# Performance work log

Measured on AMD Instinct MI355X. Metric: run time of the kernel, lower is better.

Reference implementation:

```python
import jax, jax.numpy as jnp
import numpy as np

B, T, V, H, L = 128, 512, 256, 512, 2  # batch, seq, vocab, hidden, layers


def setup_inputs() -> dict:
    key = jax.random.key(0)
    ks = jax.random.split(key, 12)
    s = 0.05
    p = lambda k, shape: (jax.random.normal(k, shape, jnp.float32) * s)
    return {
        "x": jax.random.normal(ks[0], (B, T, V), jnp.float32),
        # layer 0 (input size V)
        "w_ih0": p(ks[1], (4 * H, V)),
        "w_hh0": p(ks[2], (4 * H, H)),
        "b_ih0": p(ks[3], (4 * H,)),
        "b_hh0": p(ks[4], (4 * H,)),
        # layer 1 (input size H)
        "w_ih1": p(ks[5], (4 * H, H)),
        "w_hh1": p(ks[6], (4 * H, H)),
        "b_ih1": p(ks[7], (4 * H,)),
        "b_hh1": p(ks[8], (4 * H,)),
        # final projection
        "fc_w": p(ks[9], (V, H)),
        "fc_b": p(ks[10], (V,)),
    }


def _lstm_layer(x, w_ih, w_hh, b_ih, b_hh):
    """x: [B,T,in] -> (outputs [B,T,H], h_T [B,H], c_T [B,H]). PyTorch gate order i,f,g,o."""
    Bb = x.shape[0]
    Hh = w_hh.shape[1]
    # precompute input contribution for all timesteps: [B,T,4H]
    pre = jnp.einsum('bti,gi->btg', x, w_ih) + b_ih + b_hh

    def step(carry, xt):
        h, c = carry
        gates = xt + h @ w_hh.T  # [B,4H]
        i, f, g, o = jnp.split(gates, 4, axis=-1)
        i = jax.nn.sigmoid(i)
        f = jax.nn.sigmoid(f)
        g = jnp.tanh(g)
        o = jax.nn.sigmoid(o)
        c = f * c + i * g
        h = o * jnp.tanh(c)
        return (h, c), h

    h0 = jnp.zeros((Bb, Hh), x.dtype)
    (hT, cT), hs = jax.lax.scan(step, (h0, h0), jnp.swapaxes(pre, 0, 1))
    return jnp.swapaxes(hs, 0, 1), hT, cT


def reference(x, w_ih0, w_hh0, b_ih0, b_hh0, w_ih1, w_hh1, b_ih1, b_hh1, fc_w, fc_b):
    out0, h0, c0 = _lstm_layer(x, w_ih0, w_hh0, b_ih0, b_hh0)
    out1, h1, c1 = _lstm_layer(out0, w_ih1, w_hh1, b_ih1, b_hh1)
    last = out1[:, -1, :]                # slice final timestep [B,H]
    # dropout is identity in eval mode
    logits = last @ fc_w.T + fc_b        # [B,V]
    h_n = jnp.stack([h0, h1])            # [L,B,H]
    c_n = jnp.stack([c0, c1])
    return (logits, h_n, c_n)
```

## Files before the change

### kernel.cpp

```cpp
#include <hip/hip_runtime.h>
#include <math.h>

#define B_ 128
#define T_ 512
#define V_ 256
#define H_ 512

typedef unsigned short u16;
typedef unsigned int u32;
typedef unsigned long long u64;
typedef __attribute__((ext_vector_type(8))) __bf16 bf16x8;
typedef __attribute__((ext_vector_type(4))) float f32x4;
typedef __attribute__((ext_vector_type(4))) u32 u32x4;

__device__ __forceinline__ float sigf(float x) { return 1.f / (1.f + __expf(-x)); }
__device__ __forceinline__ float tanh_fast(float x) {
    x = fminf(fmaxf(x, -15.f), 15.f);
    float e = __expf(2.f * x);
    return (e - 1.f) / (e + 1.f);
}
__device__ __forceinline__ u16 f2bf(float f) {
    union { float f; u32 u; } v; v.f = f;
    u32 r = v.u + 0x7FFFu + ((v.u >> 16) & 1u);
    return (u16)(r >> 16);
}

__device__ __forceinline__ u64 aload(const u64* p) {
    return __hip_atomic_load(p, __ATOMIC_RELAXED, __HIP_MEMORY_SCOPE_AGENT);
}
__device__ __forceinline__ void astore(u64* p, u64 v) {
    __hip_atomic_store(p, v, __ATOMIC_RELAXED, __HIP_MEMORY_SCOPE_AGENT);
}
__device__ __forceinline__ u32 aload32(const u32* p) {
    return __hip_atomic_load(p, __ATOMIC_RELAXED, __HIP_MEMORY_SCOPE_AGENT);
}
__device__ __forceinline__ void astore32(u32* p, u32 v) {
    __hip_atomic_store(p, v, __ATOMIC_RELAXED, __HIP_MEMORY_SCOPE_AGENT);
}
__device__ __forceinline__ void pollge(const u32* slots, int idx, int target) {
    const u32* p = slots + idx;
    for (;;) {
        u32 v = aload32(p);
        if (__all((int)v >= target)) break;
        __builtin_amdgcn_s_sleep(1);
    }
    __builtin_amdgcn_sched_barrier(0);
    asm volatile("" ::: "memory");
}
__device__ __forceinline__ bf16x8 afrag(const u16* p) {
    union { u64 d[2]; bf16x8 v; } u;
    u.d[0] = aload((const u64*)p);
    u.d[1] = aload((const u64*)(p + 4));
    return u.v;
}

__global__ __launch_bounds__(256) void conv_x(u16* __restrict__ dst, const float* __restrict__ x) {
    int tid = blockIdx.x * 256 + threadIdx.x;
    int k = tid & (V_ - 1);
    int t = (tid >> 8) & (T_ - 1);
    int b = tid >> 17;
    float v = x[tid];
    int lane = (b & 15) | (((k >> 3) & 3) << 4);
    dst[((((size_t)t * 8 + (b >> 4)) * 8) + (k >> 5)) * 512 + (size_t)lane * 8 + (k & 7)] = f2bf(v);
}

__global__ __launch_bounds__(256) void conv_w(u16* __restrict__ dst,
                                              const float* __restrict__ wih,
                                              const float* __restrict__ whh,
                                              int KIN, int Ktot) {
    int tid = blockIdx.x * 256 + threadIdx.x;
    int n = tid / Ktot, k = tid - n * Ktot;
    float v = (k < KIN) ? wih[(size_t)n * KIN + k] : whh[(size_t)n * H_ + (k - KIN)];
    int lane = (n & 15) | (((k >> 3) & 3) << 4);
    dst[((size_t)((n >> 4) * (Ktot >> 5) + (k >> 5))) * 512 + (size_t)lane * 8 + (k & 7)] = f2bf(v);
}

__global__ __launch_bounds__(256) void vadd(float* __restrict__ d,
                                            const float* __restrict__ a,
                                            const float* __restrict__ b, int n) {
    int i = blockIdx.x * 256 + threadIdx.x;
    if (i < n) d[i] = a[i] + b[i];
}


template <int LAYER>
__device__ __forceinline__ void run_loop(
    const u16* __restrict__ Xswz, u16* __restrict__ Out0,
    const u16* __restrict__ WBs,
    f32x4* __restrict__ scr,
    u16* __restrict__ tileb,
    u32* __restrict__ Hgrp,
    const float* __restrict__ bsum, float* __restrict__ out,
    u32* __restrict__ bc,
    int js, int mq, int wid, int lane)
{
    constexpr int KCA = LAYER ? 16 : 8;
    constexpr int KCT = KCA + 16;
    const int m = wid & 1;
    const bool isA = wid < 2;
    const int jl = (js << 4) | (lane & 15);

    if (isA) {
        for (int s = -1; s < T_; ++s) {
            const int tc = s + 1;
            if (tc < T_) {
                f32x4 acc[4];
                #pragma unroll
                for (int g = 0; g < 4; ++g) acc[g] = (f32x4){0.f, 0.f, 0.f, 0.f};
                if (LAYER == 0) {
                    const u16* As = Xswz + (size_t)tc * 32768 + (size_t)(2 * mq + m) * 4096 + (size_t)lane * 8;
                    #pragma unroll
                    for (int kc = 0; kc < 8; ++kc) {
                        bf16x8 a = *(const bf16x8*)(As + (size_t)kc * 512);
                        #pragma unroll
                        for (int g = 0; g < 4; ++g)
                            acc[g] = __builtin_amdgcn_mfma_f32_16x16x32_bf16(
                                a, *(const bf16x8*)(WBs + (size_t)(g * KCT + kc) * 512 + (size_t)lane * 8), acc[g], 0, 0, 0);
                    }
                } else {
                    pollge(bc + m * 32, lane & 31, tc + 1);
                    const u16* As = Out0 + (size_t)tc * 65536 + (size_t)(2 * mq + m) * 8192 + (size_t)lane * 8;
                    bf16x8 fa[16];
                    #pragma unroll
                    for (int kc = 0; kc < 16; ++kc) fa[kc] = afrag(As + (size_t)kc * 512);
                    #pragma unroll
                    for (int kc = 0; kc < 16; ++kc) {
                        #pragma unroll
                        for (int g = 0; g < 4; ++g)
                            acc[g] = __builtin_amdgcn_mfma_f32_16x16x32_bf16(
                                fa[kc], *(const bf16x8*)(WBs + (size_t)(g * KCT + kc) * 512 + (size_t)lane * 8), acc[g], 0, 0, 0);
                    }
                }
                #pragma unroll
                for (int g = 0; g < 4; ++g) scr[(size_t)(((tc & 1) * 2 + m) * 4 + g) * 64 + lane] = acc[g];
            }
            __syncthreads();
        }
    } else {
        const float bi0 = bsum[jl], bi1 = bsum[512 + jl];
        const float bi2 = bsum[1024 + jl], bi3 = bsum[1536 + jl];
        f32x4 creg = {0.f, 0.f, 0.f, 0.f};
        u32* bcs = bc + m * 32 + js;

        for (int s = -1; s < T_; ++s) {
            if (s >= 0) {
                const u32 tag = (u32)s;
                const u32* hb = Hgrp + (size_t)(tag & 1) * 16384 + (size_t)m * 8192;

                f32x4 acc[4];
                #pragma unroll
                for (int g = 0; g < 4; ++g) acc[g] = scr[(size_t)(((s & 1) * 2 + m) * 4 + g) * 64 + lane];

                u64 fa[16], fb[16];
                #pragma unroll
                for (int i = 0; i < 16; ++i)
                    fa[i] = aload((const u64*)(hb + (size_t)(i >> 2) * 512 + (size_t)lane * 8) + (i & 3));

                #pragma unroll
                for (int c = 0; c < 4; ++c) {
                    u64* cur = (c & 1) ? fb : fa;
                    u64* nxt = (c & 1) ? fa : fb;
                    if (c < 3) {
                        #pragma unroll
                        for (int i = 0; i < 16; ++i)
                            nxt[i] = aload((const u64*)(hb + (size_t)((c + 1) * 4 + (i >> 2)) * 512 + (size_t)lane * 8) + (i & 3));
                    }
                    for (;;) {
                        u32 bad = 0u;
                        #pragma unroll
                        for (int i = 0; i < 16; ++i) bad |= (((u32)(cur[i] >> 16)) & 0xFFFFu) ^ tag;
                        if (!__any(bad != 0u)) break;
                        #pragma unroll
                        for (int i = 0; i < 16; ++i)
                            cur[i] = aload((const u64*)(hb + (size_t)(c * 4 + (i >> 2)) * 512 + (size_t)lane * 8) + (i & 3));
                    }
                    #pragma unroll
                    for (int k2 = 0; k2 < 4; ++k2) {
                        const u64 g0 = cur[4 * k2 + 0], g1 = cur[4 * k2 + 1];
                        const u64 g2 = cur[4 * k2 + 2], g3 = cur[4 * k2 + 3];
                        u32 w0 = (u32)(g0 & 0xFFFFu) | ((u32)(g0 >> 32) << 16);
                        u32 w1 = (u32)(g1 & 0xFFFFu) | ((u32)(g1 >> 32) << 16);
                        u32 w2 = (u32)(g2 & 0xFFFFu) | ((u32)(g2 >> 32) << 16);
                        u32 w3 = (u32)(g3 & 0xFFFFu) | ((u32)(g3 >> 32) << 16);
                        u32x4 ww = {w0, w1, w2, w3};
                        bf16x8 a = __builtin_bit_cast(bf16x8, ww);
                        const int kc = 4 * c + k2;
                        #pragma unroll
                        for (int g = 0; g < 4; ++g)
                            acc[g] = __builtin_amdgcn_mfma_f32_16x16x32_bf16(
                                a, *(const bf16x8*)(WBs + (size_t)(g * KCT + KCA + kc) * 512 + (size_t)lane * 8), acc[g], 0, 0, 0);
                    }
                }

                if (LAYER == 0 && s >= 1) {
                    asm volatile("s_waitcnt vmcnt(0)" ::: "memory");
                    if (lane == 0) astore32(bcs, (u32)s);
                }

                const bool is_last = (s == T_ - 1);
                const int bb = (lane >> 4) << 2;
                #pragma unroll
                for (int r = 0; r < 4; ++r) {
                    const float vi = sigf(acc[0][r] + bi0);
                    const float vf = sigf(acc[1][r] + bi1);
                    const float vg = tanh_fast(acc[2][r] + bi2);
                    const float vo = sigf(acc[3][r] + bi3);
                    const float cn = vf * creg[r] + vi * vg;
                    creg[r] = cn;
                    const float hn = vo * tanh_fast(cn);
                    tileb[(size_t)(m * 16 + bb + r) * 20 + (lane & 15)] = f2bf(hn);
                    if (is_last) {
                        const int bg = mq * 32 + m * 16 + bb + r;
                        out[(LAYER ? 98304 : 32768) + bg * 512 + jl] = hn;
                        out[(LAYER ? 229376 : 163840) + bg * 512 + jl] = cn;
                    }
                }
                const u32 wtag = (u32)(s + 1);
                u32* hw = Hgrp + (size_t)(wtag & 1) * 16384 + (size_t)m * 8192;
                #pragma unroll
                for (int q = 0; q < 2; ++q) {
                    u32 w = *(const u32*)&tileb[(size_t)(m * 16 + (lane >> 2)) * 20 + q * 8 + (lane & 3) * 2];
                    u64 v = (u64)(w & 0xFFFFu) | ((u64)wtag << 16)
                          | ((u64)(w >> 16) << 32) | ((u64)wtag << 48);
                    astore((u64*)(hw + (size_t)(js >> 1) * 512 + (size_t)((js & 1) * 2 + q) * 128
                                  + (size_t)(lane >> 2) * 8 + (size_t)((lane & 3) * 2)), v);
                }
                if (LAYER == 0) {
                    const int q2 = lane >> 5, lw = lane & 31, b2 = lw >> 1, e4 = (lw & 1) * 4;
                    u64 v = *(const u64*)&tileb[(size_t)(m * 16 + b2) * 20 + q2 * 8 + e4];
                    astore((u64*)(Out0 + (size_t)s * 65536 + (size_t)(2 * mq + m) * 8192
                                  + (size_t)(js >> 1) * 512 + (size_t)((js & 1) * 2 + q2) * 128
                                  + (size_t)b2 * 8 + (size_t)e4), v);
                }
            }
            __syncthreads();
        }
        if (LAYER == 0) {
            asm volatile("s_waitcnt vmcnt(0)" ::: "memory");
            if (lane == 0) astore32(bcs, (u32)(T_ + 1));
        }
    }
}

__global__ __launch_bounds__(256, 1) void lstm_persistent(
    const u16* __restrict__ Xswz, u16* __restrict__ Out0swz,
    const u16* __restrict__ WB0, const u16* __restrict__ WB1,
    const float* __restrict__ bsum0, const float* __restrict__ bsum1,
    u32* __restrict__ Htag, float* __restrict__ out, u32* __restrict__ bc)
{
    __shared__ u16 WBs[4 * 32 * 512];
    __shared__ f32x4 scr[2 * 2 * 4 * 64];
    __shared__ __align__(16) u16 tileb[2 * 16 * 20];

    const int bid = blockIdx.x;
    const int g = bid & 7, js = bid >> 3;
    const int layer = g >> 2, mq = g & 3;
    const int tid = threadIdx.x;
    const int wid = tid >> 6, lane = tid & 63;

    const int KCtot = layer ? 32 : 24;
    const u16* WB = layer ? WB1 : WB0;
    for (int gg = 0; gg < 4; ++gg) {
        const u32x4* s4 = (const u32x4*)(WB + ((size_t)(gg * 32 + js) * KCtot) * 512);
        u32x4* d4 = (u32x4*)(WBs + (size_t)gg * KCtot * 512);
        for (int i = tid; i < KCtot * 64; i += 256) d4[i] = s4[i];
    }
    __syncthreads();

    u32* Hgrp = Htag + (size_t)g * 32768;
    u32* bcg = bc + mq * 64;

    if (layer == 0)
        run_loop<0>(Xswz, Out0swz, WBs, scr, tileb, Hgrp, bsum0, out, bcg, js, mq, wid, lane);
    else
        run_loop<1>(Xswz, Out0swz, WBs, scr, tileb, Hgrp, bsum1, out, bcg, js, mq, wid, lane);
}

__device__ __forceinline__ float dot4_(float4 a, float4 w, float s) {
    s = fmaf(a.x, w.x, s); s = fmaf(a.y, w.y, s);
    s = fmaf(a.z, w.z, s); s = fmaf(a.w, w.w, s);
    return s;
}

__global__ __launch_bounds__(256) void logits_kernel(
    const float* __restrict__ h1, const float* __restrict__ fc_w,
    const float* __restrict__ fc_b, float* __restrict__ out)
{
    __shared__ float hs[H_];
    const int b = blockIdx.x;
    for (int k = threadIdx.x; k < H_; k += 256) hs[k] = h1[(size_t)b * H_ + k];
    __syncthreads();
    const int v = threadIdx.x;
    const float4* wr = reinterpret_cast<const float4*>(fc_w + (size_t)v * H_);
    const float4* hr = reinterpret_cast<const float4*>(hs);
    float s = 0.f;
    #pragma unroll 8
    for (int k = 0; k < H_ / 4; ++k) s = dot4_(hr[k], wr[k], s);
    out[(size_t)b * V_ + v] = s + fc_b[v];
}

extern "C" void kernel_launch(void* const* d_in, const int* in_sizes, int n_in,
                              void* d_out, int out_size, void* d_ws, size_t ws_size,
                              hipStream_t stream) {
    const float* x     = (const float*)d_in[0];
    const float* w_ih0 = (const float*)d_in[1];
    const float* w_hh0 = (const float*)d_in[2];
    const float* b_ih0 = (const float*)d_in[3];
    const float* b_hh0 = (const float*)d_in[4];
    const float* w_ih1 = (const float*)d_in[5];
    const float* w_hh1 = (const float*)d_in[6];
    const float* b_ih1 = (const float*)d_in[7];
    const float* b_hh1 = (const float*)d_in[8];
    const float* fc_w  = (const float*)d_in[9];
    const float* fc_b  = (const float*)d_in[10];
    float* out = (float*)d_out;

    char* p = (char*)d_ws;
    u16* Xswz    = (u16*)p; p += (size_t)512 * 32768 * 2;
    u16* Out0swz = (u16*)p; p += (size_t)512 * 65536 * 2;
    u16* WB0     = (u16*)p; p += (size_t)128 * 24 * 512 * 2;
    u16* WB1     = (u16*)p; p += (size_t)128 * 32 * 512 * 2;
    u32* Htag    = (u32*)p; p += (size_t)8 * 32768 * 4;
    float* bsum0 = (float*)p; p += 2048 * 4;
    float* bsum1 = (float*)p; p += 2048 * 4;
    u32* bc      = (u32*)p;  p += 4 * 64 * 4;

    hipMemsetAsync(Htag, 0, (size_t)8 * 32768 * 4, stream);
    hipMemsetAsync(bc, 0, 4 * 64 * 4, stream);
    conv_x<<<65536, 256, 0, stream>>>(Xswz, x);
    conv_w<<<(2048 * 768) / 256, 256, 0, stream>>>(WB0, w_ih0, w_hh0, 256, 768);
    conv_w<<<(2048 * 1024) / 256, 256, 0, stream>>>(WB1, w_ih1, w_hh1, 512, 1024);
    vadd<<<8, 256, 0, stream>>>(bsum0, b_ih0, b_hh0, 2048);
    vadd<<<8, 256, 0, stream>>>(bsum1, b_ih1, b_hh1, 2048);

    lstm_persistent<<<256, 256, 0, stream>>>(
        Xswz, Out0swz, WB0, WB1, bsum0, bsum1, Htag, out, bc);

    logits_kernel<<<B_, 256, 0, stream>>>(out + 98304, fc_w, fc_b, out);
}
```

Baseline: 2.682 ms.

## Merge input-projection waves into recurrent waves and drop per-step block barrier

Removes the separate producer waves that computed the input projection one step ahead into shared scratch, along with the __syncthreads per timestep. Each recurrent wave now computes the next step's input contribution itself, straight after storing h, so blocks shrink from 256 to 128 threads. This takes the block-wide barrier off the serial critical path. The cost is that input-projection MFMAs now run serially within each wave instead of in parallel on separate waves. The s_waitcnt before the layer-0 progress-flag store is also removed, which may weaken the ordering between the Out0 stores and the flag that layer 1 polls.

```diff
diff --git a/kernel.cpp b/kernel.cpp
--- a/kernel.cpp
+++ b/kernel.cpp
@@ -87,183 +87,186 @@
 __device__ __forceinline__ void run_loop(
     const u16* __restrict__ Xswz, u16* __restrict__ Out0,
     const u16* __restrict__ WBs,
-    f32x4* __restrict__ scr,
     u16* __restrict__ tileb,
     u32* __restrict__ Hgrp,
     const float* __restrict__ bsum, float* __restrict__ out,
     u32* __restrict__ bc,
-    int js, int mq, int wid, int lane)
+    int js, int mq, int m, int lane)
 {
     constexpr int KCA = LAYER ? 16 : 8;
     constexpr int KCT = KCA + 16;
-    const int m = wid & 1;
-    const bool isA = wid < 2;
     const int jl = (js << 4) | (lane & 15);
-
-    if (isA) {
-        for (int s = -1; s < T_; ++s) {
-            const int tc = s + 1;
-            if (tc < T_) {
-                f32x4 acc[4];
-                #pragma unroll
-                for (int g = 0; g < 4; ++g) acc[g] = (f32x4){0.f, 0.f, 0.f, 0.f};
-                if (LAYER == 0) {
-                    const u16* As = Xswz + (size_t)tc * 32768 + (size_t)(2 * mq + m) * 4096 + (size_t)lane * 8;
+    const float bi0 = bsum[jl], bi1 = bsum[512 + jl];
+    const float bi2 = bsum[1024 + jl], bi3 = bsum[1536 + jl];
+    f32x4 creg = {0.f, 0.f, 0.f, 0.f};
+    u32* bcs = bc + m * 32 + js;
+    const u32* bcp = bc + m * 32;
+
+    f32x4 acc[4];
+    #pragma unroll
+    for (int g = 0; g < 4; ++g) acc[g] = (f32x4){0.f, 0.f, 0.f, 0.f};
+
+    if (LAYER == 0) {
+        const u16* As = Xswz + (size_t)(2 * mq + m) * 4096 + (size_t)lane * 8;
+        #pragma unroll
+        for (int kc = 0; kc < 8; ++kc) {
+            bf16x8 a = *(const bf16x8*)(As + (size_t)kc * 512);
+            #pragma unroll
+            for (int g = 0; g < 4; ++g)
+                acc[g] = __builtin_amdgcn_mfma_f32_16x16x32_bf16(
+                    a, *(const bf16x8*)(WBs + (size_t)(g * KCT + kc) * 512 + (size_t)lane * 8), acc[g], 0, 0, 0);
+        }
+    } else {
+        pollge(bcp, lane & 31, 1);
+        const u16* As = Out0 + (size_t)(2 * mq + m) * 8192 + (size_t)lane * 8;
+        #pragma unroll
+        for (int kc = 0; kc < 16; ++kc) {
+            bf16x8 a = afrag(As + (size_t)kc * 512);
+            #pragma unroll
+            for (int g = 0; g < 4; ++g)
+                acc[g] = __builtin_amdgcn_mfma_f32_16x16x32_bf16(
+                    a, *(const bf16x8*)(WBs + (size_t)(g * KCT + kc) * 512 + (size_t)lane * 8), acc[g], 0, 0, 0);
+        }
+    }
+
+    for (int s = 0; s < T_; ++s) {
+        const u32 tag = (u32)s;
+        const u32* hb = Hgrp + (size_t)(s & 1) * 16384 + (size_t)m * 8192;
+        u64 fA[16], fB[16];
+        #pragma unroll
+        for (int i = 0; i < 16; ++i)
+            fA[i] = aload((const u64*)(hb + (size_t)(i >> 2) * 512 + (size_t)lane * 8) + (i & 3));
+
+        #pragma unroll
+        for (int c = 0; c < 4; ++c) {
+            u64* cur = (c & 1) ? fB : fA;
+            u64* nxt = (c & 1) ? fA : fB;
+            if (c < 3) {
+                #pragma unroll
+                for (int i = 0; i < 16; ++i)
+                    nxt[i] = aload((const u64*)(hb + (size_t)((c + 1) * 4 + (i >> 2)) * 512 + (size_t)lane * 8) + (i & 3));
+            }
+            for (;;) {
+                u32 bad = 0u;
+                #pragma unroll
+                for (int i = 0; i < 16; ++i) bad |= (((u32)(cur[i] >> 16)) & 0xFFFFu) ^ tag;
+                if (!__any(bad != 0u)) break;
+                #pragma unroll
+                for (int i = 0; i < 16; ++i)
+                    cur[i] = aload((const u64*)(hb + (size_t)(c * 4 + (i >> 2)) * 512 + (size_t)lane * 8) + (i & 3));
+            }
+            #pragma unroll
+            for (int k2 = 0; k2 < 4; ++k2) {
+                const u64 g0 = cur[4 * k2 + 0], g1 = cur[4 * k2 + 1];
+                const u64 g2 = cur[4 * k2 + 2], g3 = cur[4 * k2 + 3];
+                u32 w0 = (u32)(g0 & 0xFFFFu) | ((u32)(g0 >> 32) << 16);
+                u32 w1 = (u32)(g1 & 0xFFFFu) | ((u32)(g1 >> 32) << 16);
+                u32 w2 = (u32)(g2 & 0xFFFFu) | ((u32)(g2 >> 32) << 16);
+                u32 w3 = (u32)(g3 & 0xFFFFu) | ((u32)(g3 >> 32) << 16);
+                u32x4 ww = {w0, w1, w2, w3};
+                bf16x8 a = __builtin_bit_cast(bf16x8, ww);
+                const int kc = 4 * c + k2;
+                #pragma unroll
+                for (int g = 0; g < 4; ++g)
+                    acc[g] = __builtin_amdgcn_mfma_f32_16x16x32_bf16(
+                        a, *(const bf16x8*)(WBs + (size_t)(g * KCT + KCA + kc) * 512 + (size_t)lane * 8), acc[g], 0, 0, 0);
+            }
+        }
+
+        if (LAYER == 0 && s >= 1 && lane == 0) astore32(bcs, (u32)s);
+
+        const bool is_last = (s == T_ - 1);
+        const int bb = (lane >> 4) << 2;
+        #pragma unroll
+        for (int r = 0; r < 4; ++r) {
+            const float vi = sigf(acc[0][r] + bi0);
+            const float vf = sigf(acc[1][r] + bi1);
+            const float vg = tanh_fast(acc[2][r] + bi2);
+            const float vo = sigf(acc[3][r] + bi3);
+            const float cn = vf * creg[r] + vi * vg;
+            creg[r] = cn;
+            const float hn = vo * tanh_fast(cn);
+            tileb[(size_t)(m * 16 + bb + r) * 20 + (lane & 15)] = f2bf(hn);
+            if (is_last) {
+                const int bg = mq * 32 + m * 16 + bb + r;
+                out[(LAYER ? 98304 : 32768) + bg * 512 + jl] = hn;
+                out[(LAYER ? 229376 : 163840) + bg * 512 + jl] = cn;
+            }
+        }
+
+        const u32 wtag = (u32)(s + 1);
+        u32* hw = Hgrp + (size_t)((s + 1) & 1) * 16384 + (size_t)m * 8192;
+        #pragma unroll
+        for (int q = 0; q < 2; ++q) {
+            u32 w = *(const u32*)&tileb[(size_t)(m * 16 + (lane >> 2)) * 20 + q * 8 + (lane & 3) * 2];
+            u64 v = (u64)(w & 0xFFFFu) | ((u64)wtag << 16)
+                  | ((u64)(w >> 16) << 32) | ((u64)wtag << 48);
+            astore((u64*)(hw + (size_t)(js >> 1) * 512 + (size_t)((js & 1) * 2 + q) * 128
+                          + (size_t)(lane >> 2) * 8 + (size_t)((lane & 3) * 2)), v);
+        }
+        if (LAYER == 0) {
+            const int q2 = lane >> 5, lw = lane & 31, b2 = lw >> 1, e4 = (lw & 1) * 4;
+            u64 v = *(const u64*)&tileb[(size_t)(m * 16 + b2) * 20 + q2 * 8 + e4];
+            astore((u64*)(Out0 + (size_t)s * 65536 + (size_t)(2 * mq + m) * 8192
+                          + (size_t)(js >> 1) * 512 + (size_t)((js & 1) * 2 + q2) * 128
+                          + (size_t)b2 * 8 + (size_t)e4), v);
+        }
+
+        #pragma unroll
+        for (int g = 0; g < 4; ++g) acc[g] = (f32x4){0.f, 0.f, 0.f, 0.f};
+        if (s + 1 < T_) {
+            if (LAYER == 0) {
+                const u16* As = Xswz + (size_t)(s + 1) * 32768 + (size_t)(2 * mq + m) * 4096 + (size_t)lane * 8;
+                #pragma unroll
+                for (int kc = 0; kc < 8; ++kc) {
+                    bf16x8 a = *(const bf16x8*)(As + (size_t)kc * 512);
                     #pragma unroll
-                    for (int kc = 0; kc < 8; ++kc) {
-                        bf16x8 a = *(const bf16x8*)(As + (size_t)kc * 512);
-                        #pragma unroll
-                        for (int g = 0; g < 4; ++g)
-                            acc[g] = __builtin_amdgcn_mfma_f32_16x16x32_bf16(
-                                a, *(const bf16x8*)(WBs + (size_t)(g * KCT + kc) * 512 + (size_t)lane * 8), acc[g], 0, 0, 0);
-                    }
-                } else {
-                    pollge(bc + m * 32, lane & 31, tc + 1);
-                    const u16* As = Out0 + (size_t)tc * 65536 + (size_t)(2 * mq + m) * 8192 + (size_t)lane * 8;
-                    bf16x8 fa[16];
+                    for (int g = 0; g < 4; ++g)
+                        acc[g] = __builtin_amdgcn_mfma_f32_16x16x32_bf16(
+                            a, *(const bf16x8*)(WBs + (size_t)(g * KCT + kc) * 512 + (size_t)lane * 8), acc[g], 0, 0, 0);
+                }
+            } else {
+                pollge(bcp, lane & 31, s + 2);
+                const u16* As = Out0 + (size_t)(s + 1) * 65536 + (size_t)(2 * mq + m) * 8192 + (size_t)lane * 8;
+                #pragma unroll
+                for (int kc = 0; kc < 16; ++kc) {
+                    bf16x8 a = afrag(As + (size_t)kc * 512);
                     #pragma unroll
-                    for (int kc = 0; kc < 16; ++kc) fa[kc] = afrag(As + (size_t)kc * 512);
-                    #pragma unroll
-                    for (int kc = 0; kc < 16; ++kc) {
-                        #pragma unroll
-                        for (int g = 0; g < 4; ++g)
-                            acc[g] = __builtin_amdgcn_mfma_f32_16x16x32_bf16(
-                                fa[kc], *(const bf16x8*)(WBs + (size_t)(g * KCT + kc) * 512 + (size_t)lane * 8), acc[g], 0, 0, 0);
-                    }
+                    for (int g = 0; g < 4; ++g)
+                        acc[g] = __builtin_amdgcn_mfma_f32_16x16x32_bf16(
+                            a, *(const bf16x8*)(WBs + (size_t)(g * KCT + kc) * 512 + (size_t)lane * 8), acc[g], 0, 0, 0);
                 }
-                #pragma unroll
-                for (int g = 0; g < 4; ++g) scr[(size_t)(((tc & 1) * 2 + m) * 4 + g) * 64 + lane] = acc[g];
-            }
-            __syncthreads();
-        }
-    } else {
-        const float bi0 = bsum[jl], bi1 = bsum[512 + jl];
-        const float bi2 = bsum[1024 + jl], bi3 = bsum[1536 + jl];
-        f32x4 creg = {0.f, 0.f, 0.f, 0.f};
-        u32* bcs = bc + m * 32 + js;
-
-        for (int s = -1; s < T_; ++s) {
-            if (s >= 0) {
-                const u32 tag = (u32)s;
-                const u32* hb = Hgrp + (size_t)(tag & 1) * 16384 + (size_t)m * 8192;
-
-                f32x4 acc[4];
-                #pragma unroll
-                for (int g = 0; g < 4; ++g) acc[g] = scr[(size_t)(((s & 1) * 2 + m) * 4 + g) * 64 + lane];
-
-                u64 fa[16], fb[16];
-                #pragma unroll
-                for (int i = 0; i < 16; ++i)
-                    fa[i] = aload((const u64*)(hb + (size_t)(i >> 2) * 512 + (size_t)lane * 8) + (i & 3));
-
-                #pragma unroll
-                for (int c = 0; c < 4; ++c) {
-                    u64* cur = (c & 1) ? fb : fa;
-                    u64* nxt = (c & 1) ? fa : fb;
-                    if (c < 3) {
-                        #pragma unroll
-                        for (int i = 0; i < 16; ++i)
-                            nxt[i] = aload((const u64*)(hb + (size_t)((c + 1) * 4 + (i >> 2)) * 512 + (size_t)lane * 8) + (i & 3));
-                    }
-                    for (;;) {
-                        u32 bad = 0u;
-                        #pragma unroll
-                        for (int i = 0; i < 16; ++i) bad |= (((u32)(cur[i] >> 16)) & 0xFFFFu) ^ tag;
-                        if (!__any(bad != 0u)) break;
-                        #pragma unroll
-                        for (int i = 0; i < 16; ++i)
-                            cur[i] = aload((const u64*)(hb + (size_t)(c * 4 + (i >> 2)) * 512 + (size_t)lane * 8) + (i & 3));
-                    }
-                    #pragma unroll
-                    for (int k2 = 0; k2 < 4; ++k2) {
-                        const u64 g0 = cur[4 * k2 + 0], g1 = cur[4 * k2 + 1];
-                        const u64 g2 = cur[4 * k2 + 2], g3 = cur[4 * k2 + 3];
-                        u32 w0 = (u32)(g0 & 0xFFFFu) | ((u32)(g0 >> 32) << 16);
-                        u32 w1 = (u32)(g1 & 0xFFFFu) | ((u32)(g1 >> 32) << 16);
-                        u32 w2 = (u32)(g2 & 0xFFFFu) | ((u32)(g2 >> 32) << 16);
-                        u32 w3 = (u32)(g3 & 0xFFFFu) | ((u32)(g3 >> 32) << 16);
-                        u32x4 ww = {w0, w1, w2, w3};
-                        bf16x8 a = __builtin_bit_cast(bf16x8, ww);
-                        const int kc = 4 * c + k2;
-                        #pragma unroll
-                        for (int g = 0; g < 4; ++g)
-                            acc[g] = __builtin_amdgcn_mfma_f32_16x16x32_bf16(
-                                a, *(const bf16x8*)(WBs + (size_t)(g * KCT + KCA + kc) * 512 + (size_t)lane * 8), acc[g], 0, 0, 0);
-                    }
-                }
-
-                if (LAYER == 0 && s >= 1) {
-                    asm volatile("s_waitcnt vmcnt(0)" ::: "memory");
-                    if (lane == 0) astore32(bcs, (u32)s);
-                }
-
-                const bool is_last = (s == T_ - 1);
-                const int bb = (lane >> 4) << 2;
-                #pragma unroll
-                for (int r = 0; r < 4; ++r) {
-                    const float vi = sigf(acc[0][r] + bi0);
-                    const float vf = sigf(acc[1][r] + bi1);
-                    const float vg = tanh_fast(acc[2][r] + bi2);
-                    const float vo = sigf(acc[3][r] + bi3);
-                    const float cn = vf * creg[r] + vi * vg;
-                    creg[r] = cn;
-                    const float hn = vo * tanh_fast(cn);
-                    tileb[(size_t)(m * 16 + bb + r) * 20 + (lane & 15)] = f2bf(hn);
-                    if (is_last) {
-                        const int bg = mq * 32 + m * 16 + bb + r;
-                        out[(LAYER ? 98304 : 32768) + bg * 512 + jl] = hn;
-                        out[(LAYER ? 229376 : 163840) + bg * 512 + jl] = cn;
-                    }
-                }
-                const u32 wtag = (u32)(s + 1);
-                u32* hw = Hgrp + (size_t)(wtag & 1) * 16384 + (size_t)m * 8192;
-                #pragma unroll
-                for (int q = 0; q < 2; ++q) {
-                    u32 w = *(const u32*)&tileb[(size_t)(m * 16 + (lane >> 2)) * 20 + q * 8 + (lane & 3) * 2];
-                    u64 v = (u64)(w & 0xFFFFu) | ((u64)wtag << 16)
-                          | ((u64)(w >> 16) << 32) | ((u64)wtag << 48);
-                    astore((u64*)(hw + (size_t)(js >> 1) * 512 + (size_t)((js & 1) * 2 + q) * 128
-                                  + (size_t)(lane >> 2) * 8 + (size_t)((lane & 3) * 2)), v);
-                }
-                if (LAYER == 0) {
-                    const int q2 = lane >> 5, lw = lane & 31, b2 = lw >> 1, e4 = (lw & 1) * 4;
-                    u64 v = *(const u64*)&tileb[(size_t)(m * 16 + b2) * 20 + q2 * 8 + e4];
-                    astore((u64*)(Out0 + (size_t)s * 65536 + (size_t)(2 * mq + m) * 8192
-                                  + (size_t)(js >> 1) * 512 + (size_t)((js & 1) * 2 + q2) * 128
-                                  + (size_t)b2 * 8 + (size_t)e4), v);
-                }
-            }
-            __syncthreads();
-        }
-        if (LAYER == 0) {
-            asm volatile("s_waitcnt vmcnt(0)" ::: "memory");
-            if (lane == 0) astore32(bcs, (u32)(T_ + 1));
-        }
-    }
-}
-
-__global__ __launch_bounds__(256, 1) void lstm_persistent(
+            }
+        }
+    }
+
+    if (LAYER == 0) {
+        asm volatile("s_waitcnt vmcnt(0)" ::: "memory");
+        if (lane == 0) astore32(bcs, (u32)(T_ + 1));
+    }
+}
+
+__global__ __launch_bounds__(128, 1) void lstm_persistent(
     const u16* __restrict__ Xswz, u16* __restrict__ Out0swz,
     const u16* __restrict__ WB0, const u16* __restrict__ WB1,
     const float* __restrict__ bsum0, const float* __restrict__ bsum1,
     u32* __restrict__ Htag, float* __restrict__ out, u32* __restrict__ bc)
 {
     __shared__ u16 WBs[4 * 32 * 512];
-    __shared__ f32x4 scr[2 * 2 * 4 * 64];
     __shared__ __align__(16) u16 tileb[2 * 16 * 20];
 
     const int bid = blockIdx.x;
     const int g = bid & 7, js = bid >> 3;
     const int layer = g >> 2, mq = g & 3;
     const int tid = threadIdx.x;
-    const int wid = tid >> 6, lane = tid & 63;
+    const int m = tid >> 6, lane = tid & 63;
 
     const int KCtot = layer ? 32 : 24;
     const u16* WB = layer ? WB1 : WB0;
     for (int gg = 0; gg < 4; ++gg) {
         const u32x4* s4 = (const u32x4*)(WB + ((size_t)(gg * 32 + js) * KCtot) * 512);
         u32x4* d4 = (u32x4*)(WBs + (size_t)gg * KCtot * 512);
-        for (int i = tid; i < KCtot * 64; i += 256) d4[i] = s4[i];
+        for (int i = tid; i < KCtot * 64; i += 128) d4[i] = s4[i];
     }
     __syncthreads();
 
@@ -271,9 +274,9 @@
     u32* bcg = bc + mq * 64;
 
     if (layer == 0)
-        run_loop<0>(Xswz, Out0swz, WBs, scr, tileb, Hgrp, bsum0, out, bcg, js, mq, wid, lane);
+        run_loop<0>(Xswz, Out0swz, WBs, tileb, Hgrp, bsum0, out, bcg, js, mq, m, lane);
     else
-        run_loop<1>(Xswz, Out0swz, WBs, scr, tileb, Hgrp, bsum1, out, bcg, js, mq, wid, lane);
+        run_loop<1>(Xswz, Out0swz, WBs, tileb, Hgrp, bsum1, out, bcg, js, mq, m, lane);
 }
 
 __device__ __forceinline__ float dot4_(float4 a, float4 w, float s) {
@@ -333,7 +336,7 @@
     vadd<<<8, 256, 0, stream>>>(bsum0, b_ih0, b_hh0, 2048);
     vadd<<<8, 256, 0, stream>>>(bsum1, b_ih1, b_hh1, 2048);
 
-    lstm_persistent<<<256, 256, 0, stream>>>(
+    lstm_persistent<<<256, 128, 0, stream>>>(
         Xswz, Out0swz, WB0, WB1, bsum0, bsum1, Htag, out, bc);
 
     logits_kernel<<<B_, 256, 0, stream>>>(out + 98304, fc_w, fc_b, out);
```

Measured after the change: 5.098 ms. 1.9x slower.

## Replace block-wide barriers with LDS mailbox flags between producer and consumer waves

Applied to the files above, without the earlier changes.

The per-timestep __syncthreads that coupled the input-projection waves and the recurrent waves is replaced by LDS mailbox counters. Each producer/consumer pair now handshakes point-to-point through a two-slot buffer, which lets the input projection run up to one step ahead without stalling all four waves. The recurrent waves also issue their first h loads before waiting on the mailbox, and the vmcnt wait before the layer-0 progress store is removed. The risks are spin-wait overhead and memory-ordering hazards, since the progress flag can now be published before the Out0 stores have completed.

```diff
diff --git a/kernel.cpp b/kernel.cpp
--- a/kernel.cpp
+++ b/kernel.cpp
@@ -89,6 +89,7 @@
     const u16* __restrict__ WBs,
     f32x4* __restrict__ scr,
     u16* __restrict__ tileb,
+    volatile u32* __restrict__ mbox,
     u32* __restrict__ Hgrp,
     const float* __restrict__ bsum, float* __restrict__ out,
     u32* __restrict__ bc,
@@ -101,40 +102,42 @@
     const int jl = (js << 4) | (lane & 15);
 
     if (isA) {
-        for (int s = -1; s < T_; ++s) {
-            const int tc = s + 1;
-            if (tc < T_) {
-                f32x4 acc[4];
+        for (int tc = 0; tc < T_; ++tc) {
+            while ((int)mbox[2 + m] < tc - 1) __builtin_amdgcn_s_sleep(1);
+            __builtin_amdgcn_sched_barrier(0);
+            asm volatile("" ::: "memory");
+
+            f32x4 acc[4];
+            #pragma unroll
+            for (int g = 0; g < 4; ++g) acc[g] = (f32x4){0.f, 0.f, 0.f, 0.f};
+            if (LAYER == 0) {
+                const u16* As = Xswz + (size_t)tc * 32768 + (size_t)(2 * mq + m) * 4096 + (size_t)lane * 8;
                 #pragma unroll
-                for (int g = 0; g < 4; ++g) acc[g] = (f32x4){0.f, 0.f, 0.f, 0.f};
-                if (LAYER == 0) {
-                    const u16* As = Xswz + (size_t)tc * 32768 + (size_t)(2 * mq + m) * 4096 + (size_t)lane * 8;
-                    #pragma unroll
-                    for (int kc = 0; kc < 8; ++kc) {
-                        bf16x8 a = *(const bf16x8*)(As + (size_t)kc * 512);
-                        #pragma unroll
-                        for (int g = 0; g < 4; ++g)
-                            acc[g] = __builtin_amdgcn_mfma_f32_16x16x32_bf16(
-                                a, *(const bf16x8*)(WBs + (size_t)(g * KCT + kc) * 512 + (size_t)lane * 8), acc[g], 0, 0, 0);
-                    }
-                } else {
-                    pollge(bc + m * 32, lane & 31, tc + 1);
-                    const u16* As = Out0 + (size_t)tc * 65536 + (size_t)(2 * mq + m) * 8192 + (size_t)lane * 8;
-                    bf16x8 fa[16];
-                    #pragma unroll
-                    for (int kc = 0; kc < 16; ++kc) fa[kc] = afrag(As + (size_t)kc * 512);
-                    #pragma unroll
-                    for (int kc = 0; kc < 16; ++kc) {
-                        #pragma unroll
-                        for (int g = 0; g < 4; ++g)
-                            acc[g] = __builtin_amdgcn_mfma_f32_16x16x32_bf16(
-                                fa[kc], *(const bf16x8*)(WBs + (size_t)(g * KCT + kc) * 512 + (size_t)lane * 8), acc[g], 0, 0, 0);
-                    }
-                }
+                for (int kc = 0; kc < 8; ++kc) {
+                    bf16x8 a = *(const bf16x8*)(As + (size_t)kc * 512);
+                    #pragma unroll
+                    for (int g = 0; g < 4; ++g)
+                        acc[g] = __builtin_amdgcn_mfma_f32_16x16x32_bf16(
+                            a, *(const bf16x8*)(WBs + (size_t)(g * KCT + kc) * 512 + (size_t)lane * 8), acc[g], 0, 0, 0);
+                }
+            } else {
+                pollge(bc + m * 32, lane & 31, tc + 1);
+                const u16* As = Out0 + (size_t)tc * 65536 + (size_t)(2 * mq + m) * 8192 + (size_t)lane * 8;
+                bf16x8 fa[16];
                 #pragma unroll
-                for (int g = 0; g < 4; ++g) scr[(size_t)(((tc & 1) * 2 + m) * 4 + g) * 64 + lane] = acc[g];
-            }
-            __syncthreads();
+                for (int kc = 0; kc < 16; ++kc) fa[kc] = afrag(As + (size_t)kc * 512);
+                #pragma unroll
+                for (int kc = 0; kc < 16; ++kc) {
+                    #pragma unroll
+                    for (int g = 0; g < 4; ++g)
+                        acc[g] = __builtin_amdgcn_mfma_f32_16x16x32_bf16(
+                            fa[kc], *(const bf16x8*)(WBs + (size_t)(g * KCT + kc) * 512 + (size_t)lane * 8), acc[g], 0, 0, 0);
+                }
+            }
+            #pragma unroll
+            for (int g = 0; g < 4; ++g) scr[(size_t)(((tc & 1) * 2 + m) * 4 + g) * 64 + lane] = acc[g];
+            asm volatile("s_waitcnt lgkmcnt(0)" ::: "memory");
+            if (lane == 0) mbox[m] = (u32)(tc + 1);
         }
     } else {
         const float bi0 = bsum[jl], bi1 = bsum[512 + jl];
@@ -142,98 +145,96 @@
         f32x4 creg = {0.f, 0.f, 0.f, 0.f};
         u32* bcs = bc + m * 32 + js;
 
-        for (int s = -1; s < T_; ++s) {
-            if (s >= 0) {
-                const u32 tag = (u32)s;
-                const u32* hb = Hgrp + (size_t)(tag & 1) * 16384 + (size_t)m * 8192;
-
-                f32x4 acc[4];
+        for (int s = 0; s < T_; ++s) {
+            const u32 tag = (u32)s;
+            const u32* hb = Hgrp + (size_t)(s & 1) * 16384 + (size_t)m * 8192;
+            u64 fA[16], fB[16];
+            #pragma unroll
+            for (int i = 0; i < 16; ++i)
+                fA[i] = aload((const u64*)(hb + (size_t)(i >> 2) * 512 + (size_t)lane * 8) + (i & 3));
+
+            while ((int)mbox[m] < s + 1) __builtin_amdgcn_s_sleep(1);
+            __builtin_amdgcn_sched_barrier(0);
+            asm volatile("" ::: "memory");
+            f32x4 acc[4];
+            #pragma unroll
+            for (int g = 0; g < 4; ++g) acc[g] = scr[(size_t)(((s & 1) * 2 + m) * 4 + g) * 64 + lane];
+            asm volatile("s_waitcnt lgkmcnt(0)" ::: "memory");
+            if (lane == 0) mbox[2 + m] = (u32)(s + 1);
+
+            #pragma unroll
+            for (int c = 0; c < 4; ++c) {
+                u64* cur = (c & 1) ? fB : fA;
+                u64* nxt = (c & 1) ? fA : fB;
+                if (c < 3) {
+                    #pragma unroll
+                    for (int i = 0; i < 16; ++i)
+                        nxt[i] = aload((const u64*)(hb + (size_t)((c + 1) * 4 + (i >> 2)) * 512 + (size_t)lane * 8) + (i & 3));
+                }
+                for (;;) {
+                    u32 bad = 0u;
+                    #pragma unroll
+                    for (int i = 0; i < 16; ++i) bad |= (((u32)(cur[i] >> 16)) & 0xFFFFu) ^ tag;
+                    if (!__any(bad != 0u)) break;
+                    #pragma unroll
+                    for (int i = 0; i < 16; ++i)
+                        cur[i] = aload((const u64*)(hb + (size_t)(c * 4 + (i >> 2)) * 512 + (size_t)lane * 8) + (i & 3));
+                }
                 #pragma unroll
-                for (int g = 0; g < 4; ++g) acc[g] = scr[(size_t)(((s & 1) * 2 + m) * 4 + g) * 64 + lane];
-
-                u64 fa[16], fb[16];
-                #pragma unroll
-                for (int i = 0; i < 16; ++i)
-                    fa[i] = aload((const u64*)(hb + (size_t)(i >> 2) * 512 + (size_t)lane * 8) + (i & 3));
-
-                #pragma unroll
-                for (int c = 0; c < 4; ++c) {
-                    u64* cur = (c & 1) ? fb : fa;
-                    u64* nxt = (c & 1) ? fa : fb;
-                    if (c < 3) {
-                        #pragma unroll
-                        for (int i = 0; i < 16; ++i)
-                            nxt[i] = aload((const u64*)(hb + (size_t)((c + 1) * 4 + (i >> 2)) * 512 + (size_t)lane * 8) + (i & 3));
-                    }
-                    for (;;) {
-                        u32 bad = 0u;
-                        #pragma unroll
-                        for (int i = 0; i < 16; ++i) bad |= (((u32)(cur[i] >> 16)) & 0xFFFFu) ^ tag;
-                        if (!__any(bad != 0u)) break;
-                        #pragma unroll
-                        for (int i = 0; i < 16; ++i)
-                            cur[i] = aload((const u64*)(hb + (size_t)(c * 4 + (i >> 2)) * 512 + (size_t)lane * 8) + (i & 3));
-                    }
-                    #pragma unroll
-                    for (int k2 = 0; k2 < 4; ++k2) {
-                        const u64 g0 = cur[4 * k2 + 0], g1 = cur[4 * k2 + 1];
-                        const u64 g2 = cur[4 * k2 + 2], g3 = cur[4 * k2 + 3];
-                        u32 w0 = (u32)(g0 & 0xFFFFu) | ((u32)(g0 >> 32) << 16);
-                        u32 w1 = (u32)(g1 & 0xFFFFu) | ((u32)(g1 >> 32) << 16);
-                        u32 w2 = (u32)(g2 & 0xFFFFu) | ((u32)(g2 >> 32) << 16);
-                        u32 w3 = (u32)(g3 & 0xFFFFu) | ((u32)(g3 >> 32) << 16);
-                        u32x4 ww = {w0, w1, w2, w3};
-                        bf16x8 a = __builtin_bit_cast(bf16x8, ww);
-                        const int kc = 4 * c + k2;
-                        #pragma unroll
-                        for (int g = 0; g < 4; ++g)
-                            acc[g] = __builtin_amdgcn_mfma_f32_16x16x32_bf16(
-                                a, *(const bf16x8*)(WBs + (size_t)(g * KCT + KCA + kc) * 512 + (size_t)lane * 8), acc[g], 0, 0, 0);
-                    }
-                }
-
-                if (LAYER == 0 && s >= 1) {
-                    asm volatile("s_waitcnt vmcnt(0)" ::: "memory");
-                    if (lane == 0) astore32(bcs, (u32)s);
-                }
-
-                const bool is_last = (s == T_ - 1);
-                const int bb = (lane >> 4) << 2;
-                #pragma unroll
-                for (int r = 0; r < 4; ++r) {
-                    const float vi = sigf(acc[0][r] + bi0);
-                    const float vf = sigf(acc[1][r] + bi1);
-                    const float vg = tanh_fast(acc[2][r] + bi2);
-                    const float vo = sigf(acc[3][r] + bi3);
-                    const float cn = vf * creg[r] + vi * vg;
-                    creg[r] = cn;
-                    const float hn = vo * tanh_fast(cn);
-                    tileb[(size_t)(m * 16 + bb + r) * 20 + (lane & 15)] = f2bf(hn);
-                    if (is_last) {
-                        const int bg = mq * 32 + m * 16 + bb + r;
-                        out[(LAYER ? 98304 : 32768) + bg * 512 + jl] = hn;
-                        out[(LAYER ? 229376 : 163840) + bg * 512 + jl] = cn;
-                    }
-                }
-                const u32 wtag = (u32)(s + 1);
-                u32* hw = Hgrp + (size_t)(wtag & 1) * 16384 + (size_t)m * 8192;
-                #pragma unroll
-                for (int q = 0; q < 2; ++q) {
-                    u32 w = *(const u32*)&tileb[(size_t)(m * 16 + (lane >> 2)) * 20 + q * 8 + (lane & 3) * 2];
-                    u64 v = (u64)(w & 0xFFFFu) | ((u64)wtag << 16)
-                          | ((u64)(w >> 16) << 32) | ((u64)wtag << 48);
-                    astore((u64*)(hw + (size_t)(js >> 1) * 512 + (size_t)((js & 1) * 2 + q) * 128
-                                  + (size_t)(lane >> 2) * 8 + (size_t)((lane & 3) * 2)), v);
-                }
-                if (LAYER == 0) {
-                    const int q2 = lane >> 5, lw = lane & 31, b2 = lw >> 1, e4 = (lw & 1) * 4;
-                    u64 v = *(const u64*)&tileb[(size_t)(m * 16 + b2) * 20 + q2 * 8 + e4];
-                    astore((u64*)(Out0 + (size_t)s * 65536 + (size_t)(2 * mq + m) * 8192
-                                  + (size_t)(js >> 1) * 512 + (size_t)((js & 1) * 2 + q2) * 128
-                                  + (size_t)b2 * 8 + (size_t)e4), v);
-                }
-            }
-            __syncthreads();
+                for (int k2 = 0; k2 < 4; ++k2) {
+                    const u64 g0 = cur[4 * k2 + 0], g1 = cur[4 * k2 + 1];
+                    const u64 g2 = cur[4 * k2 + 2], g3 = cur[4 * k2 + 3];
+                    u32 w0 = (u32)(g0 & 0xFFFFu) | ((u32)(g0 >> 32) << 16);
+                    u32 w1 = (u32)(g1 & 0xFFFFu) | ((u32)(g1 >> 32) << 16);
+                    u32 w2 = (u32)(g2 & 0xFFFFu) | ((u32)(g2 >> 32) << 16);
+                    u32 w3 = (u32)(g3 & 0xFFFFu) | ((u32)(g3 >> 32) << 16);
+                    u32x4 ww = {w0, w1, w2, w3};
+                    bf16x8 a = __builtin_bit_cast(bf16x8, ww);
+                    const int kc = 4 * c + k2;
+                    #pragma unroll
+                    for (int g = 0; g < 4; ++g)
+                        acc[g] = __builtin_amdgcn_mfma_f32_16x16x32_bf16(
+                            a, *(const bf16x8*)(WBs + (size_t)(g * KCT + KCA + kc) * 512 + (size_t)lane * 8), acc[g], 0, 0, 0);
+                }
+            }
+
+            if (LAYER == 0 && s >= 1 && lane == 0) astore32(bcs, (u32)s);
+
+            const bool is_last = (s == T_ - 1);
+            const int bb = (lane >> 4) << 2;
+            #pragma unroll
+            for (int r = 0; r < 4; ++r) {
+                const float vi = sigf(acc[0][r] + bi0);
+                const float vf = sigf(acc[1][r] + bi1);
+                const float vg = tanh_fast(acc[2][r] + bi2);
+                const float vo = sigf(acc[3][r] + bi3);
+                const float cn = vf * creg[r] + vi * vg;
+                creg[r] = cn;
+                const float hn = vo * tanh_fast(cn);
+                tileb[(size_t)(m * 16 + bb + r) * 20 + (lane & 15)] = f2bf(hn);
+                if (is_last) {
+                    const int bg = mq * 32 + m * 16 + bb + r;
+                    out[(LAYER ? 98304 : 32768) + bg * 512 + jl] = hn;
+                    out[(LAYER ? 229376 : 163840) + bg * 512 + jl] = cn;
+                }
+            }
+            const u32 wtag = (u32)(s + 1);
+            u32* hw = Hgrp + (size_t)((s + 1) & 1) * 16384 + (size_t)m * 8192;
+            #pragma unroll
+            for (int q = 0; q < 2; ++q) {
+                u32 w = *(const u32*)&tileb[(size_t)(m * 16 + (lane >> 2)) * 20 + q * 8 + (lane & 3) * 2];
+                u64 v = (u64)(w & 0xFFFFu) | ((u64)wtag << 16)
+                      | ((u64)(w >> 16) << 32) | ((u64)wtag << 48);
+                astore((u64*)(hw + (size_t)(js >> 1) * 512 + (size_t)((js & 1) * 2 + q) * 128
+                              + (size_t)(lane >> 2) * 8 + (size_t)((lane & 3) * 2)), v);
+            }
+            if (LAYER == 0) {
+                const int q2 = lane >> 5, lw = lane & 31, b2 = lw >> 1, e4 = (lw & 1) * 4;
+                u64 v = *(const u64*)&tileb[(size_t)(m * 16 + b2) * 20 + q2 * 8 + e4];
+                astore((u64*)(Out0 + (size_t)s * 65536 + (size_t)(2 * mq + m) * 8192
+                              + (size_t)(js >> 1) * 512 + (size_t)((js & 1) * 2 + q2) * 128
+                              + (size_t)b2 * 8 + (size_t)e4), v);
+            }
         }
         if (LAYER == 0) {
             asm volatile("s_waitcnt vmcnt(0)" ::: "memory");
@@ -251,6 +252,7 @@
     __shared__ u16 WBs[4 * 32 * 512];
     __shared__ f32x4 scr[2 * 2 * 4 * 64];
     __shared__ __align__(16) u16 tileb[2 * 16 * 20];
+    __shared__ u32 mbox[4];
 
     const int bid = blockIdx.x;
     const int g = bid & 7, js = bid >> 3;
@@ -265,15 +267,16 @@
         u32x4* d4 = (u32x4*)(WBs + (size_t)gg * KCtot * 512);
         for (int i = tid; i < KCtot * 64; i += 256) d4[i] = s4[i];
     }
+    if (tid < 4) mbox[tid] = 0u;
     __syncthreads();
 
     u32* Hgrp = Htag + (size_t)g * 32768;
     u32* bcg = bc + mq * 64;
 
     if (layer == 0)
-        run_loop<0>(Xswz, Out0swz, WBs, scr, tileb, Hgrp, bsum0, out, bcg, js, mq, wid, lane);
+        run_loop<0>(Xswz, Out0swz, WBs, scr, tileb, mbox, Hgrp, bsum0, out, bcg, js, mq, wid, lane);
     else
-        run_loop<1>(Xswz, Out0swz, WBs, scr, tileb, Hgrp, bsum1, out, bcg, js, mq, wid, lane);
+        run_loop<1>(Xswz, Out0swz, WBs, scr, tileb, mbox, Hgrp, bsum1, out, bcg, js, mq, wid, lane);
 }
 
 __device__ __forceinline__ float dot4_(float4 a, float4 w, float s) {
```

After: 3.132 ms. 16.8% more time.

## Use 64-slot hidden-state ring with vector loads and lazy atomic retry polling

Applied to the files above, without the earlier changes.

The hidden-state exchange buffer grows from double-buffered to a 64-slot ring. The first read of each chunk now uses plain 128-bit vector loads, and the slower atomic reload loop with s_sleep runs only when a tag check fails. The vmcnt(0) wait before the layer-0 progress signal is removed. The aim is to cut polling and load latency on the per-step critical path. In exchange, the workspace and the memset grow, plain loads may read stale cached data, and dropping the wait may weaken the ordering guarantee behind the progress counter.

```diff
diff --git a/kernel.cpp b/kernel.cpp
--- a/kernel.cpp
+++ b/kernel.cpp
@@ -5,6 +5,7 @@
 #define T_ 512
 #define V_ 256
 #define H_ 512
+#define RING_ 64
 
 typedef unsigned short u16;
 typedef unsigned int u32;
@@ -145,43 +146,57 @@
         for (int s = -1; s < T_; ++s) {
             if (s >= 0) {
                 const u32 tag = (u32)s;
-                const u32* hb = Hgrp + (size_t)(tag & 1) * 16384 + (size_t)m * 8192;
+                const u32* hb = Hgrp + (size_t)(s & (RING_ - 1)) * 16384 + (size_t)m * 8192;
 
                 f32x4 acc[4];
                 #pragma unroll
                 for (int g = 0; g < 4; ++g) acc[g] = scr[(size_t)(((s & 1) * 2 + m) * 4 + g) * 64 + lane];
 
-                u64 fa[16], fb[16];
-                #pragma unroll
-                for (int i = 0; i < 16; ++i)
-                    fa[i] = aload((const u64*)(hb + (size_t)(i >> 2) * 512 + (size_t)lane * 8) + (i & 3));
+                u32x4 vA[8], vB[8];
+                #pragma unroll
+                for (int i = 0; i < 8; ++i)
+                    vA[i] = *(const u32x4*)(hb + (size_t)(i >> 1) * 512 + (size_t)lane * 8 + (size_t)(i & 1) * 4);
 
                 #pragma unroll
                 for (int c = 0; c < 4; ++c) {
-                    u64* cur = (c & 1) ? fb : fa;
-                    u64* nxt = (c & 1) ? fa : fb;
+                    u32x4* cur = (c & 1) ? vB : vA;
+                    u32x4* nxt = (c & 1) ? vA : vB;
                     if (c < 3) {
                         #pragma unroll
-                        for (int i = 0; i < 16; ++i)
-                            nxt[i] = aload((const u64*)(hb + (size_t)((c + 1) * 4 + (i >> 2)) * 512 + (size_t)lane * 8) + (i & 3));
-                    }
-                    for (;;) {
-                        u32 bad = 0u;
-                        #pragma unroll
-                        for (int i = 0; i < 16; ++i) bad |= (((u32)(cur[i] >> 16)) & 0xFFFFu) ^ tag;
-                        if (!__any(bad != 0u)) break;
-                        #pragma unroll
-                        for (int i = 0; i < 16; ++i)
-                            cur[i] = aload((const u64*)(hb + (size_t)(c * 4 + (i >> 2)) * 512 + (size_t)lane * 8) + (i & 3));
+                        for (int i = 0; i < 8; ++i)
+                            nxt[i] = *(const u32x4*)(hb + (size_t)((c + 1) * 4 + (i >> 1)) * 512 + (size_t)lane * 8 + (size_t)(i & 1) * 4);
+                    }
+                    u32 bad = 0u;
+                    #pragma unroll
+                    for (int i = 0; i < 8; ++i)
+                        bad |= ((cur[i][0] >> 16) ^ tag) | ((cur[i][1] >> 16) ^ tag)
+                             | ((cur[i][2] >> 16) ^ tag) | ((cur[i][3] >> 16) ^ tag);
+                    if (__any(bad != 0u)) {
+                        for (;;) {
+                            #pragma unroll
+                            for (int i = 0; i < 8; ++i) {
+                                const u64* p = (const u64*)(hb + (size_t)(c * 4 + (i >> 1)) * 512
+                                                            + (size_t)lane * 8 + (size_t)(i & 1) * 4);
+                                u64 lo = aload(p), hi = aload(p + 1);
+                                cur[i][0] = (u32)lo; cur[i][1] = (u32)(lo >> 32);
+                                cur[i][2] = (u32)hi; cur[i][3] = (u32)(hi >> 32);
+                            }
+                            u32 b2 = 0u;
+                            #pragma unroll
+                            for (int i = 0; i < 8; ++i)
+                                b2 |= ((cur[i][0] >> 16) ^ tag) | ((cur[i][1] >> 16) ^ tag)
+                                    | ((cur[i][2] >> 16) ^ tag) | ((cur[i][3] >> 16) ^ tag);
+                            if (!__any(b2 != 0u)) break;
+                            __builtin_amdgcn_s_sleep(1);
+                        }
                     }
                     #pragma unroll
                     for (int k2 = 0; k2 < 4; ++k2) {
-                        const u64 g0 = cur[4 * k2 + 0], g1 = cur[4 * k2 + 1];
-                        const u64 g2 = cur[4 * k2 + 2], g3 = cur[4 * k2 + 3];
-                        u32 w0 = (u32)(g0 & 0xFFFFu) | ((u32)(g0 >> 32) << 16);
-                        u32 w1 = (u32)(g1 & 0xFFFFu) | ((u32)(g1 >> 32) << 16);
-                        u32 w2 = (u32)(g2 & 0xFFFFu) | ((u32)(g2 >> 32) << 16);
-                        u32 w3 = (u32)(g3 & 0xFFFFu) | ((u32)(g3 >> 32) << 16);
+                        u32x4 a0 = cur[2 * k2], a1 = cur[2 * k2 + 1];
+                        u32 w0 = (a0[0] & 0xFFFFu) | (a0[1] << 16);
+                        u32 w1 = (a0[2] & 0xFFFFu) | (a0[3] << 16);
+                        u32 w2 = (a1[0] & 0xFFFFu) | (a1[1] << 16);
+                        u32 w3 = (a1[2] & 0xFFFFu) | (a1[3] << 16);
                         u32x4 ww = {w0, w1, w2, w3};
                         bf16x8 a = __builtin_bit_cast(bf16x8, ww);
                         const int kc = 4 * c + k2;
@@ -192,10 +207,7 @@
                     }
                 }
 
-                if (LAYER == 0 && s >= 1) {
-                    asm volatile("s_waitcnt vmcnt(0)" ::: "memory");
-                    if (lane == 0) astore32(bcs, (u32)s);
-                }
+                if (LAYER == 0 && s >= 1 && lane == 0) astore32(bcs, (u32)s);
 
                 const bool is_last = (s == T_ - 1);
                 const int bb = (lane >> 4) << 2;
@@ -216,7 +228,7 @@
                     }
                 }
                 const u32 wtag = (u32)(s + 1);
-                u32* hw = Hgrp + (size_t)(wtag & 1) * 16384 + (size_t)m * 8192;
+                u32* hw = Hgrp + (size_t)((s + 1) & (RING_ - 1)) * 16384 + (size_t)m * 8192;
                 #pragma unroll
                 for (int q = 0; q < 2; ++q) {
                     u32 w = *(const u32*)&tileb[(size_t)(m * 16 + (lane >> 2)) * 20 + q * 8 + (lane & 3) * 2];
@@ -267,7 +279,7 @@
     }
     __syncthreads();
 
-    u32* Hgrp = Htag + (size_t)g * 32768;
+    u32* Hgrp = Htag + (size_t)g * (RING_ * 16384);
     u32* bcg = bc + mq * 64;
 
     if (layer == 0)
@@ -320,12 +332,12 @@
     u16* Out0swz = (u16*)p; p += (size_t)512 * 65536 * 2;
     u16* WB0     = (u16*)p; p += (size_t)128 * 24 * 512 * 2;
     u16* WB1     = (u16*)p; p += (size_t)128 * 32 * 512 * 2;
-    u32* Htag    = (u32*)p; p += (size_t)8 * 32768 * 4;
+    u32* Htag    = (u32*)p; p += (size_t)8 * RING_ * 16384 * 4;
     float* bsum0 = (float*)p; p += 2048 * 4;
     float* bsum1 = (float*)p; p += 2048 * 4;
     u32* bc      = (u32*)p;  p += 4 * 64 * 4;
 
-    hipMemsetAsync(Htag, 0, (size_t)8 * 32768 * 4, stream);
+    hipMemsetAsync(Htag, 0, (size_t)8 * RING_ * 16384 * 4, stream);
     hipMemsetAsync(bc, 0, 4 * 64 * 4, stream);
     conv_x<<<65536, 256, 0, stream>>>(Xswz, x);
     conv_w<<<(2048 * 768) / 256, 256, 0, stream>>>(WB0, w_ih0, w_hh0, 256, 768);
```

Result: slower. 2.749 ms (+2.5%).
